# Performance work log

Hardware: AMD Instinct MI355X
Metric: run time of the kernel (lower is better)

The kernel has to match this reference:

```python
import jax, jax.numpy as jnp
import numpy as np

EPS = 1e-6

def _ln(x, g, b):
    m = jnp.mean(x, axis=-1, keepdims=True)
    v = jnp.mean(jnp.square(x - m), axis=-1, keepdims=True)
    return (x - m) * jax.lax.rsqrt(v + EPS) * g + b

def _pw(x, w, b):
    # 1x1 conv == channel matmul. x: [B,H,W,Ci], w: [Ci,Co]
    return jnp.einsum('bhwc,co->bhwo', x, w) + b

def _dw3x3(x, w, b):
    # depthwise 3x3, SAME. x: [B,H,W,C], w: [3,3,1,C]
    c = x.shape[-1]
    y = jax.lax.conv_general_dilated(
        x, w, window_strides=(1, 1), padding='SAME',
        dimension_numbers=('NHWC', 'HWIO', 'NHWC'),
        feature_group_count=c)
    return y + b

def setup_inputs() -> dict:
    key = jax.random.key(0)
    ks = jax.random.split(key, 16)
    B, H, W, C = 8, 256, 256, 64
    hid = C * 2            # channels * expansion
    s = lambda *sh: 0.02
    inp = {
        'x':     jax.random.normal(ks[0], (B, H, W, C), jnp.float32),
        'ln1_g': jnp.ones((C,), jnp.float32),
        'ln1_b': jnp.zeros((C,), jnp.float32),
        'pw1_w': jax.random.normal(ks[1], (C, hid * 2), jnp.float32) * 0.05,
        'pw1_b': jnp.zeros((hid * 2,), jnp.float32),
        'dw_w':  jax.random.normal(ks[2], (3, 3, 1, hid * 2), jnp.float32) * 0.05,
        'dw_b':  jnp.zeros((hid * 2,), jnp.float32),
        'sca_w': jax.random.normal(ks[3], (hid, hid), jnp.float32) * 0.05,
        'sca_b': jnp.zeros((hid,), jnp.float32),
        'pw2_w': jax.random.normal(ks[4], (hid, C), jnp.float32) * 0.05,
        'pw2_b': jnp.zeros((C,), jnp.float32),
        'beta':  jax.random.normal(ks[5], (1, 1, 1, C), jnp.float32) * 0.1,
        'ln2_g': jnp.ones((C,), jnp.float32),
        'ln2_b': jnp.zeros((C,), jnp.float32),
        'pw3_w': jax.random.normal(ks[6], (C, hid * 2), jnp.float32) * 0.05,
        'pw3_b': jnp.zeros((hid * 2,), jnp.float32),
        'pw4_w': jax.random.normal(ks[7], (hid, C), jnp.float32) * 0.05,
        'pw4_b': jnp.zeros((C,), jnp.float32),
        'gamma': jax.random.normal(ks[8], (1, 1, 1, C), jnp.float32) * 0.1,
    }
    return inp

def reference(x, ln1_g, ln1_b, pw1_w, pw1_b, dw_w, dw_b, sca_w, sca_b,
              pw2_w, pw2_b, beta, ln2_g, ln2_b, pw3_w, pw3_b, pw4_w, pw4_b, gamma):
    # ---- stage 1: norm -> pw1 -> dw3x3 -> SimpleGate -> SCA -> pw2 -> scaled residual
    y = _ln(x, ln1_g, ln1_b)
    y = _pw(y, pw1_w, pw1_b)            # [B,H,W,2*hid]
    y = _dw3x3(y, dw_w, dw_b)
    y1, y2 = jnp.split(y, 2, axis=-1)
    y = y1 * y2                          # SimpleGate -> [B,H,W,hid]
    w = jnp.mean(y, axis=(1, 2), keepdims=True)          # GAP [B,1,1,hid]
    w = _pw(w, sca_w, sca_b)             # 1x1 conv on pooled stats
    y = y * w                            # channel attention
    y = _pw(y, pw2_w, pw2_b)             # [B,H,W,C]
    x = x + y * beta
    # ---- stage 2: norm -> pw3 -> SimpleGate -> pw4 -> scaled residual
    z = _ln(x, ln2_g, ln2_b)
    z = _pw(z, pw3_w, pw3_b)             # [B,H,W,2*hid]
    z1, z2 = jnp.split(z, 2, axis=-1)
    z = z1 * z2                          # [B,H,W,hid]
    z = _pw(z, pw4_w, pw4_b)             # [B,H,W,C]
    return x + z * gamma
```

## Files before the change

kernel.cpp:

```cpp
#include <hip/hip_runtime.h>

typedef __attribute__((ext_vector_type(8))) _Float16 f16x8;
typedef __attribute__((ext_vector_type(2))) _Float16 h2;
typedef __attribute__((ext_vector_type(4))) float f32x4;
typedef __attribute__((ext_vector_type(2))) float f32x2;
typedef __attribute__((ext_vector_type(4))) unsigned uint4_t;
typedef __attribute__((ext_vector_type(2))) unsigned uint2_t;

__device__ __forceinline__ h2 pkrtz(float a, float b) {
    return __builtin_bit_cast(h2, __builtin_amdgcn_cvt_pkrtz(a, b));
}
__device__ __forceinline__ unsigned h2u(h2 v) { return __builtin_bit_cast(unsigned, v); }
__device__ __forceinline__ h2 u2h(unsigned u) { return __builtin_bit_cast(h2, u); }
__device__ __forceinline__ short f2h(float f) { return __builtin_bit_cast(short, (_Float16)f); }

#define OFF_W1T 0L
#define OFF_W2T 32768L
#define OFF_W3T 49152L
#define OFF_W4T 81920L
#define OFF_DWH 98304L
#define OFF_DBH 102912L
#define OFF_WATT 103424L
#define OFF_GPART 107520L
#define OFF_T 1156096L

__global__ __launch_bounds__(256) void k_prep(
    const float* __restrict__ w1, const float* __restrict__ w2,
    const float* __restrict__ w3, const float* __restrict__ w4,
    const float* __restrict__ dww, const float* __restrict__ dwb,
    short* __restrict__ w1t, short* __restrict__ w2t,
    short* __restrict__ w3t, short* __restrict__ w4t,
    short* __restrict__ dwh, short* __restrict__ dbh)
{
    int id = blockIdx.x * 256 + threadIdx.x;
    if (id < 64 * 256) {
        int ci = id >> 8, co = id & 255;
        w1t[co * 64 + ci] = f2h(w1[id]);
        w3t[co * 64 + ci] = f2h(w3[id]);
    }
    if (id < 128 * 64) {
        int ci = id >> 6, co = id & 63;
        w2t[co * 128 + ci] = f2h(w2[id]);
        w4t[co * 128 + ci] = f2h(w4[id]);
    }
    if (id < 9 * 256) dwh[id] = f2h(dww[id]);
    if (id < 256)     dbh[id] = f2h(dwb[id]);
}

__global__ __launch_bounds__(256) void k_a(
    const float* __restrict__ x, const float* __restrict__ ln1g, const float* __restrict__ ln1b,
    const short* __restrict__ w1t, const float* __restrict__ b1,
    const short* __restrict__ dwh, const short* __restrict__ dbh,
    short* __restrict__ t)
{
    __shared__ short uh[100 * 128];
    const int blk = blockIdx.x;
    const int cs  = blk & 1;
    const int txy = blk >> 1;
    const int tx  = txy & 31;
    const int ty  = (txy >> 5) & 31;
    const int b   = txy >> 10;
    const int tid = threadIdx.x;
    const int lane = tid & 63;
    const int wave = tid >> 6;
    const int m    = lane & 15;
    const int quad = lane >> 4;

    const int pA = wave * 16 + m;
    const int pB = pA + 64;
    const int hyA = (pA * 205) >> 11, hxA = pA - hyA * 10;
    const int hyB = (pB * 205) >> 11, hxB = pB - hyB * 10;
    const int gyA = ty * 8 + hyA - 1, gxA = tx * 8 + hxA - 1;
    const int gyB = ty * 8 + hyB - 1, gxB = tx * 8 + hxB - 1;
    const bool imgA = gyA >= 0 && gyA < 256 && gxA >= 0 && gxA < 256;
    const bool imgB = (pB < 100) && gyB >= 0 && gyB < 256 && gxB >= 0 && gxB < 256;
    const bool aliveB = (wave < 3);

    f32x4 fA[4], fB[4];
#pragma unroll
    for (int i = 0; i < 4; ++i) {
        fA[i] = (f32x4){0.f,0.f,0.f,0.f};
        fB[i] = (f32x4){0.f,0.f,0.f,0.f};
    }
    if (imgA) {
        const float* xr = x + ((long)((b * 256 + gyA) * 256 + gxA)) * 64 + quad * 8;
        fA[0] = *(const f32x4*)(xr);      fA[1] = *(const f32x4*)(xr + 4);
        fA[2] = *(const f32x4*)(xr + 32); fA[3] = *(const f32x4*)(xr + 36);
    }
    if (imgB) {
        const float* xr = x + ((long)((b * 256 + gyB) * 256 + gxB)) * 64 + quad * 8;
        fB[0] = *(const f32x4*)(xr);      fB[1] = *(const f32x4*)(xr + 4);
        fB[2] = *(const f32x4*)(xr + 32); fB[3] = *(const f32x4*)(xr + 36);
    }

    f32x4 g0 = *(const f32x4*)(ln1g + quad * 8);
    f32x4 g1 = *(const f32x4*)(ln1g + quad * 8 + 4);
    f32x4 g2 = *(const f32x4*)(ln1g + 32 + quad * 8);
    f32x4 g3 = *(const f32x4*)(ln1g + 32 + quad * 8 + 4);
    f32x4 c0 = *(const f32x4*)(ln1b + quad * 8);
    f32x4 c1 = *(const f32x4*)(ln1b + quad * 8 + 4);
    f32x4 c2 = *(const f32x4*)(ln1b + 32 + quad * 8);
    f32x4 c3 = *(const f32x4*)(ln1b + 32 + quad * 8 + 4);

    f16x8 a0A = {0,0,0,0,0,0,0,0}, a1A = {0,0,0,0,0,0,0,0};
    f16x8 a0B = {0,0,0,0,0,0,0,0}, a1B = {0,0,0,0,0,0,0,0};

    if (imgA) {
        float s  = 0.f, s2 = 0.f;
#pragma unroll
        for (int i = 0; i < 4; ++i)
#pragma unroll
            for (int r = 0; r < 4; ++r) { s += fA[i][r]; s2 += fA[i][r] * fA[i][r]; }
        s  += __shfl_xor(s, 16);  s  += __shfl_xor(s, 32);
        s2 += __shfl_xor(s2, 16); s2 += __shfl_xor(s2, 32);
        float mean = s * 0.015625f;
        float var  = s2 * 0.015625f - mean * mean;
        float rs   = rsqrtf(var + 1e-6f);
        float mrs  = mean * rs;
        uint4_t ra, rb;
#define LNP(va,vb,ga,gb,ca,cb) h2u(pkrtz(((va)*rs - mrs)*(ga) + (ca), ((vb)*rs - mrs)*(gb) + (cb)))
        ra[0] = LNP(fA[0][0],fA[0][1],g0[0],g0[1],c0[0],c0[1]);
        ra[1] = LNP(fA[0][2],fA[0][3],g0[2],g0[3],c0[2],c0[3]);
        ra[2] = LNP(fA[1][0],fA[1][1],g1[0],g1[1],c1[0],c1[1]);
        ra[3] = LNP(fA[1][2],fA[1][3],g1[2],g1[3],c1[2],c1[3]);
        rb[0] = LNP(fA[2][0],fA[2][1],g2[0],g2[1],c2[0],c2[1]);
        rb[1] = LNP(fA[2][2],fA[2][3],g2[2],g2[3],c2[2],c2[3]);
        rb[2] = LNP(fA[3][0],fA[3][1],g3[0],g3[1],c3[0],c3[1]);
        rb[3] = LNP(fA[3][2],fA[3][3],g3[2],g3[3],c3[2],c3[3]);
        a0A = __builtin_bit_cast(f16x8, ra);
        a1A = __builtin_bit_cast(f16x8, rb);
    }
    if (imgB) {
        float s  = 0.f, s2 = 0.f;
#pragma unroll
        for (int i = 0; i < 4; ++i)
#pragma unroll
            for (int r = 0; r < 4; ++r) { s += fB[i][r]; s2 += fB[i][r] * fB[i][r]; }
        s  += __shfl_xor(s, 16);  s  += __shfl_xor(s, 32);
        s2 += __shfl_xor(s2, 16); s2 += __shfl_xor(s2, 32);
        float mean = s * 0.015625f;
        float var  = s2 * 0.015625f - mean * mean;
        float rs   = rsqrtf(var + 1e-6f);
        float mrs  = mean * rs;
        uint4_t ra, rb;
        ra[0] = LNP(fB[0][0],fB[0][1],g0[0],g0[1],c0[0],c0[1]);
        ra[1] = LNP(fB[0][2],fB[0][3],g0[2],g0[3],c0[2],c0[3]);
        ra[2] = LNP(fB[1][0],fB[1][1],g1[0],g1[1],c1[0],c1[1]);
        ra[3] = LNP(fB[1][2],fB[1][3],g1[2],g1[3],c1[2],c1[3]);
        rb[0] = LNP(fB[2][0],fB[2][1],g2[0],g2[1],c2[0],c2[1]);
        rb[1] = LNP(fB[2][2],fB[2][3],g2[2],g2[3],c2[2],c2[3]);
        rb[2] = LNP(fB[3][0],fB[3][1],g3[0],g3[1],c3[0],c3[1]);
        rb[3] = LNP(fB[3][2],fB[3][3],g3[2],g3[3],c3[2],c3[3]);
#undef LNP
        a0B = __builtin_bit_cast(f16x8, ra);
        a1B = __builtin_bit_cast(f16x8, rb);
    }

    char* uhc = (char*)uh;
#pragma unroll
    for (int cot = 0; cot < 8; ++cot) {
        const int cob = (cot < 4) ? (cs * 64 + cot * 16) : (128 + cs * 64 + (cot - 4) * 16);
        const f16x8 wlo = __builtin_bit_cast(f16x8, *(const uint4_t*)(w1t + (cob + m) * 64 + quad * 8));
        const f16x8 whi = __builtin_bit_cast(f16x8, *(const uint4_t*)(w1t + (cob + m) * 64 + 32 + quad * 8));
        const f32x4 bv = *(const f32x4*)(b1 + cob + quad * 4);
        {
            f32x4 acc = {0.f,0.f,0.f,0.f};
            acc = __builtin_amdgcn_mfma_f32_16x16x32_f16(wlo, a0A, acc, 0, 0, 0);
            acc = __builtin_amdgcn_mfma_f32_16x16x32_f16(whi, a1A, acc, 0, 0, 0);
            uint2_t pk;
            pk[0] = imgA ? h2u(pkrtz(acc[0] + bv[0], acc[1] + bv[1])) : 0u;
            pk[1] = imgA ? h2u(pkrtz(acc[2] + bv[2], acc[3] + bv[3])) : 0u;
            int off = (pA * 256 + cot * 32 + quad * 8) ^ ((pA & 7) << 4);
            *(uint2_t*)(uhc + off) = pk;
        }
        if (aliveB) {
            f32x4 acc = {0.f,0.f,0.f,0.f};
            acc = __builtin_amdgcn_mfma_f32_16x16x32_f16(wlo, a0B, acc, 0, 0, 0);
            acc = __builtin_amdgcn_mfma_f32_16x16x32_f16(whi, a1B, acc, 0, 0, 0);
            if (pB < 100) {
                uint2_t pk;
                pk[0] = imgB ? h2u(pkrtz(acc[0] + bv[0], acc[1] + bv[1])) : 0u;
                pk[1] = imgB ? h2u(pkrtz(acc[2] + bv[2], acc[3] + bv[3])) : 0u;
                int off = (pB * 256 + cot * 32 + quad * 8) ^ ((pB & 7) << 4);
                *(uint2_t*)(uhc + off) = pk;
            }
        }
    }
    __syncthreads();

    const int y = lane >> 3, xx = lane & 7;
    const int cq = wave;
    const int gc0 = cs * 64 + cq * 16;
    const long gpx = ((long)(b * 256 + ty * 8 + y) * 256) + tx * 8 + xx;

    h2 A1[8], A2[8];
#pragma unroll
    for (int j = 0; j < 8; ++j) {
        A1[j] = u2h(0u);
        A2[j] = u2h(0u);
    }
#pragma unroll
    for (int dy = 0; dy < 3; ++dy)
#pragma unroll
    for (int dx = 0; dx < 3; ++dx) {
        int h = (y + dy) * 10 + (xx + dx);
        int sw = (h & 7) << 4;
        int b0 = h * 256 + cq * 32;
        uint4_t u1l  = *(const uint4_t*)(uhc + ((b0)       ^ sw));
        uint4_t u1h  = *(const uint4_t*)(uhc + ((b0 + 16)  ^ sw));
        uint4_t u2l  = *(const uint4_t*)(uhc + ((b0 + 128) ^ sw));
        uint4_t u2hv = *(const uint4_t*)(uhc + ((b0 + 144) ^ sw));
        const uint4_t* wp = (const uint4_t*)(dwh + (dy * 3 + dx) * 256 + gc0);
        const uint4_t* vp = (const uint4_t*)(dwh + (dy * 3 + dx) * 256 + 128 + gc0);
        uint4_t w1l = wp[0], w1h = wp[1];
        uint4_t w2l = vp[0], w2h = vp[1];
#pragma unroll
        for (int j = 0; j < 4; ++j) {
            A1[j]     += u2h(u1l[j])  * u2h(w1l[j]);
            A1[j + 4] += u2h(u1h[j])  * u2h(w1h[j]);
            A2[j]     += u2h(u2l[j])  * u2h(w2l[j]);
            A2[j + 4] += u2h(u2hv[j]) * u2h(w2h[j]);
        }
    }
    const uint4_t* bp1 = (const uint4_t*)(dbh + gc0);
    const uint4_t* bp2 = (const uint4_t*)(dbh + 128 + gc0);
    uint4_t b1l = bp1[0], b1h = bp1[1];
    uint4_t b2l = bp2[0], b2h = bp2[1];
    uint4_t s0, s1;
#pragma unroll
    for (int j = 0; j < 4; ++j) {
        h2 t0 = (A1[j]     + u2h(b1l[j])) * (A2[j]     + u2h(b2l[j]));
        h2 t1 = (A1[j + 4] + u2h(b1h[j])) * (A2[j + 4] + u2h(b2h[j]));
        s0[j] = h2u(t0);
        s1[j] = h2u(t1);
    }
    *(uint4_t*)(t + gpx * 128 + gc0)     = s0;
    *(uint4_t*)(t + gpx * 128 + gc0 + 8) = s1;
}

__global__ __launch_bounds__(256) void k_red(
    const short* __restrict__ t, float* __restrict__ gpart)
{
    __shared__ float red[16][16][8];
    const int blk = blockIdx.x;
    const int tid = threadIdx.x;
    const int cg = tid & 15;
    const int pr = tid >> 4;
    const short* tb = t + (long)blk * 256 * 128 + cg * 8;
    float a0=0,a1=0,a2=0,a3=0,a4=0,a5=0,a6=0,a7=0;
#pragma unroll 4
    for (int it = 0; it < 16; ++it) {
        uint4_t u = *(const uint4_t*)(tb + (long)(it * 16 + pr) * 128);
        h2 v0=u2h(u[0]), v1=u2h(u[1]), v2=u2h(u[2]), v3=u2h(u[3]);
        a0 += (float)v0[0]; a1 += (float)v0[1]; a2 += (float)v1[0]; a3 += (float)v1[1];
        a4 += (float)v2[0]; a5 += (float)v2[1]; a6 += (float)v3[0]; a7 += (float)v3[1];
    }
    red[pr][cg][0]=a0; red[pr][cg][1]=a1; red[pr][cg][2]=a2; red[pr][cg][3]=a3;
    red[pr][cg][4]=a4; red[pr][cg][5]=a5; red[pr][cg][6]=a6; red[pr][cg][7]=a7;
    __syncthreads();
    if (tid < 128) {
        int g = tid >> 3, j = tid & 7;
        float s = 0.f;
#pragma unroll
        for (int r = 0; r < 16; ++r) s += red[r][g][j];
        gpart[(long)blk * 128 + tid] = s;
    }
}

__global__ __launch_bounds__(256) void k_sca2(
    const float* __restrict__ gpart, const float* __restrict__ scaw,
    const float* __restrict__ scab, float* __restrict__ watt)
{
    __shared__ float gl[256];
    __shared__ float gn[128];
    const int b = blockIdx.x;
    const int tid = threadIdx.x;
    const int c = tid & 127, half = tid >> 7;
    float s = 0.f;
    const float* gp = gpart + (long)b * 256 * 128 + c;
    for (int i = half; i < 256; i += 2) s += gp[(long)i * 128];
    gl[half * 128 + c] = s;
    __syncthreads();
    if (tid < 128) gn[c] = (gl[c] + gl[128 + c]) * (1.0f / 65536.0f);
    __syncthreads();
    if (tid < 128) {
        float acc = scab[c];
        for (int ci = 0; ci < 128; ++ci) acc += gn[ci] * scaw[ci * 128 + c];
        watt[b * 128 + c] = acc;
    }
}

#define XLST 72
#define ZTST 136
__global__ __launch_bounds__(256) void k_b(
    const short* __restrict__ t, const float* __restrict__ watt,
    const short* __restrict__ w2t, const float* __restrict__ b2,
    const float* __restrict__ x, const float* __restrict__ beta,
    const float* __restrict__ ln2g, const float* __restrict__ ln2b,
    const short* __restrict__ w3t, const float* __restrict__ b3,
    const short* __restrict__ w4t, const float* __restrict__ b4,
    const float* __restrict__ gamma, float* __restrict__ out)
{
    __shared__ short xl[8][16 * XLST];
    __shared__ short zt[8][16 * ZTST];
    const int lane = threadIdx.x & 63;
    const int wave = threadIdx.x >> 6;
    const int m = lane & 15, quad = lane >> 4;
    const long pxA = (long)blockIdx.x * 128 + wave * 16 + m;
    const long pxB = pxA + 64;
    const int b = (int)(((long)blockIdx.x * 128) >> 16);
    const float* wa = watt + b * 128;
    const int sA = wave, sB = wave + 4;

    f32x4 xvA[4], xvB[4];
#pragma unroll
    for (int nt = 0; nt < 4; ++nt) {
        xvA[nt] = *(const f32x4*)(x + pxA * 64 + nt * 16 + quad * 4);
        xvB[nt] = *(const f32x4*)(x + pxB * 64 + nt * 16 + quad * 4);
    }

    const short* trA = t + pxA * 128;
    const short* trB = t + pxB * 128;
    f32x4 acc2A[4], acc2B[4];
#pragma unroll
    for (int nt = 0; nt < 4; ++nt) {
        acc2A[nt] = (f32x4){0.f,0.f,0.f,0.f};
        acc2B[nt] = (f32x4){0.f,0.f,0.f,0.f};
    }
#pragma unroll
    for (int kh = 0; kh < 4; ++kh) {
        uint4_t tA = *(const uint4_t*)(trA + kh * 32 + quad * 8);
        uint4_t tB = *(const uint4_t*)(trB + kh * 32 + quad * 8);
        f32x4 w0  = *(const f32x4*)(wa + kh * 32 + quad * 8);
        f32x4 w1v = *(const f32x4*)(wa + kh * 32 + quad * 8 + 4);
        h2 s01 = pkrtz(w0[0], w0[1]),  s23 = pkrtz(w0[2], w0[3]);
        h2 s45 = pkrtz(w1v[0], w1v[1]), s67 = pkrtz(w1v[2], w1v[3]);
        uint4_t oA, oB;
        oA[0] = h2u(u2h(tA[0]) * s01); oA[1] = h2u(u2h(tA[1]) * s23);
        oA[2] = h2u(u2h(tA[2]) * s45); oA[3] = h2u(u2h(tA[3]) * s67);
        oB[0] = h2u(u2h(tB[0]) * s01); oB[1] = h2u(u2h(tB[1]) * s23);
        oB[2] = h2u(u2h(tB[2]) * s45); oB[3] = h2u(u2h(tB[3]) * s67);
        f16x8 bfrA = __builtin_bit_cast(f16x8, oA);
        f16x8 bfrB = __builtin_bit_cast(f16x8, oB);
#pragma unroll
        for (int nt = 0; nt < 4; ++nt) {
            f16x8 aw = __builtin_bit_cast(f16x8,
                *(const uint4_t*)(w2t + (nt * 16 + m) * 128 + kh * 32 + quad * 8));
            acc2A[nt] = __builtin_amdgcn_mfma_f32_16x16x32_f16(aw, bfrA, acc2A[nt], 0, 0, 0);
            acc2B[nt] = __builtin_amdgcn_mfma_f32_16x16x32_f16(aw, bfrB, acc2B[nt], 0, 0, 0);
        }
    }
    float x1A[4][4], x1B[4][4];
#pragma unroll
    for (int nt = 0; nt < 4; ++nt) {
        int cob = nt * 16 + quad * 4;
        f32x4 bb = *(const f32x4*)(b2 + cob);
        f32x4 be = *(const f32x4*)(beta + cob);
#pragma unroll
        for (int r = 0; r < 4; ++r) {
            x1A[nt][r] = xvA[nt][r] + (acc2A[nt][r] + bb[r]) * be[r];
            x1B[nt][r] = xvB[nt][r] + (acc2B[nt][r] + bb[r]) * be[r];
        }
    }
    float sa = 0.f, s2a = 0.f, sb = 0.f, s2b = 0.f;
#pragma unroll
    for (int nt = 0; nt < 4; ++nt)
#pragma unroll
        for (int r = 0; r < 4; ++r) {
            sa += x1A[nt][r]; s2a += x1A[nt][r] * x1A[nt][r];
            sb += x1B[nt][r]; s2b += x1B[nt][r] * x1B[nt][r];
        }
    sa  += __shfl_xor(sa, 16);  sa  += __shfl_xor(sa, 32);
    s2a += __shfl_xor(s2a, 16); s2a += __shfl_xor(s2a, 32);
    sb  += __shfl_xor(sb, 16);  sb  += __shfl_xor(sb, 32);
    s2b += __shfl_xor(s2b, 16); s2b += __shfl_xor(s2b, 32);
    float meanA = sa * 0.015625f;
    float varA  = s2a * 0.015625f - meanA * meanA;
    float rsA   = rsqrtf(varA + 1e-6f);
    float mrsA  = meanA * rsA;
    float meanB = sb * 0.015625f;
    float varB  = s2b * 0.015625f - meanB * meanB;
    float rsB   = rsqrtf(varB + 1e-6f);
    float mrsB  = meanB * rsB;
#pragma unroll
    for (int nt = 0; nt < 4; ++nt) {
        int cob = nt * 16 + quad * 4;
        f32x4 gg = *(const f32x4*)(ln2g + cob);
        f32x4 cc = *(const f32x4*)(ln2b + cob);
        uint2_t pkA, pkB;
        pkA[0] = h2u(pkrtz((x1A[nt][0] * rsA - mrsA) * gg[0] + cc[0],
                           (x1A[nt][1] * rsA - mrsA) * gg[1] + cc[1]));
        pkA[1] = h2u(pkrtz((x1A[nt][2] * rsA - mrsA) * gg[2] + cc[2],
                           (x1A[nt][3] * rsA - mrsA) * gg[3] + cc[3]));
        pkB[0] = h2u(pkrtz((x1B[nt][0] * rsB - mrsB) * gg[0] + cc[0],
                           (x1B[nt][1] * rsB - mrsB) * gg[1] + cc[1]));
        pkB[1] = h2u(pkrtz((x1B[nt][2] * rsB - mrsB) * gg[2] + cc[2],
                           (x1B[nt][3] * rsB - mrsB) * gg[3] + cc[3]));
        *(uint2_t*)&xl[sA][m * XLST + cob] = pkA;
        *(uint2_t*)&xl[sB][m * XLST + cob] = pkB;
    }
    f16x8 xbA0 = __builtin_bit_cast(f16x8, *(const uint4_t*)&xl[sA][m * XLST + quad * 8]);
    f16x8 xbA1 = __builtin_bit_cast(f16x8, *(const uint4_t*)&xl[sA][m * XLST + 32 + quad * 8]);
    f16x8 xbB0 = __builtin_bit_cast(f16x8, *(const uint4_t*)&xl[sB][m * XLST + quad * 8]);
    f16x8 xbB1 = __builtin_bit_cast(f16x8, *(const uint4_t*)&xl[sB][m * XLST + 32 + quad * 8]);
#pragma unroll
    for (int pg = 0; pg < 8; ++pg) {
        f16x8 w3a0 = __builtin_bit_cast(f16x8, *(const uint4_t*)(w3t + (pg * 16 + m) * 64 + quad * 8));
        f16x8 w3a1 = __builtin_bit_cast(f16x8, *(const uint4_t*)(w3t + (pg * 16 + m) * 64 + 32 + quad * 8));
        f16x8 w3b0 = __builtin_bit_cast(f16x8, *(const uint4_t*)(w3t + (128 + pg * 16 + m) * 64 + quad * 8));
        f16x8 w3b1 = __builtin_bit_cast(f16x8, *(const uint4_t*)(w3t + (128 + pg * 16 + m) * 64 + 32 + quad * 8));
        f32x4 aAA = {0.f,0.f,0.f,0.f}, aBA = {0.f,0.f,0.f,0.f};
        f32x4 aAB = {0.f,0.f,0.f,0.f}, aBB = {0.f,0.f,0.f,0.f};
        aAA = __builtin_amdgcn_mfma_f32_16x16x32_f16(w3a0, xbA0, aAA, 0, 0, 0);
        aAA = __builtin_amdgcn_mfma_f32_16x16x32_f16(w3a1, xbA1, aAA, 0, 0, 0);
        aBA = __builtin_amdgcn_mfma_f32_16x16x32_f16(w3b0, xbA0, aBA, 0, 0, 0);
        aBA = __builtin_amdgcn_mfma_f32_16x16x32_f16(w3b1, xbA1, aBA, 0, 0, 0);
        aAB = __builtin_amdgcn_mfma_f32_16x16x32_f16(w3a0, xbB0, aAB, 0, 0, 0);
        aAB = __builtin_amdgcn_mfma_f32_16x16x32_f16(w3a1, xbB1, aAB, 0, 0, 0);
        aBB = __builtin_amdgcn_mfma_f32_16x16x32_f16(w3b0, xbB0, aBB, 0, 0, 0);
        aBB = __builtin_amdgcn_mfma_f32_16x16x32_f16(w3b1, xbB1, aBB, 0, 0, 0);
        int cb = pg * 16 + quad * 4;
        f32x4 bA_ = *(const f32x4*)(b3 + cb);
        f32x4 bB_ = *(const f32x4*)(b3 + 128 + cb);
        uint2_t pkA, pkB;
        pkA[0] = h2u(pkrtz((aAA[0] + bA_[0]) * (aBA[0] + bB_[0]),
                           (aAA[1] + bA_[1]) * (aBA[1] + bB_[1])));
        pkA[1] = h2u(pkrtz((aAA[2] + bA_[2]) * (aBA[2] + bB_[2]),
                           (aAA[3] + bA_[3]) * (aBA[3] + bB_[3])));
        pkB[0] = h2u(pkrtz((aAB[0] + bA_[0]) * (aBB[0] + bB_[0]),
                           (aAB[1] + bA_[1]) * (aBB[1] + bB_[1])));
        pkB[1] = h2u(pkrtz((aAB[2] + bA_[2]) * (aBB[2] + bB_[2]),
                           (aAB[3] + bA_[3]) * (aBB[3] + bB_[3])));
        *(uint2_t*)&zt[sA][m * ZTST + cb] = pkA;
        *(uint2_t*)&zt[sB][m * ZTST + cb] = pkB;
    }
    f32x4 acc4A[4], acc4B[4];
#pragma unroll
    for (int nt = 0; nt < 4; ++nt) {
        acc4A[nt] = (f32x4){0.f,0.f,0.f,0.f};
        acc4B[nt] = (f32x4){0.f,0.f,0.f,0.f};
    }
#pragma unroll
    for (int kh = 0; kh < 4; ++kh) {
        f16x8 zbA = __builtin_bit_cast(f16x8, *(const uint4_t*)&zt[sA][m * ZTST + kh * 32 + quad * 8]);
        f16x8 zbB = __builtin_bit_cast(f16x8, *(const uint4_t*)&zt[sB][m * ZTST + kh * 32 + quad * 8]);
#pragma unroll
        for (int nt = 0; nt < 4; ++nt) {
            f16x8 aw = __builtin_bit_cast(f16x8,
                *(const uint4_t*)(w4t + (nt * 16 + m) * 128 + kh * 32 + quad * 8));
            acc4A[nt] = __builtin_amdgcn_mfma_f32_16x16x32_f16(aw, zbA, acc4A[nt], 0, 0, 0);
            acc4B[nt] = __builtin_amdgcn_mfma_f32_16x16x32_f16(aw, zbB, acc4B[nt], 0, 0, 0);
        }
    }
#pragma unroll
    for (int nt = 0; nt < 4; ++nt) {
        int cob = nt * 16 + quad * 4;
        f32x4 bb = *(const f32x4*)(b4 + cob);
        f32x4 gm = *(const f32x4*)(gamma + cob);
        f32x4 oA, oB;
#pragma unroll
        for (int r = 0; r < 4; ++r) {
            oA[r] = x1A[nt][r] + (acc4A[nt][r] + bb[r]) * gm[r];
            oB[r] = x1B[nt][r] + (acc4B[nt][r] + bb[r]) * gm[r];
        }
        *(f32x4*)(out + pxA * 64 + cob) = oA;
        *(f32x4*)(out + pxB * 64 + cob) = oB;
    }
}

extern "C" void kernel_launch(void* const* d_in, const int* in_sizes, int n_in,
                              void* d_out, int out_size, void* d_ws, size_t ws_size,
                              hipStream_t stream) {
    (void)in_sizes; (void)n_in; (void)out_size; (void)ws_size;
    const float* x    = (const float*)d_in[0];
    const float* ln1g = (const float*)d_in[1];
    const float* ln1b = (const float*)d_in[2];
    const float* pw1w = (const float*)d_in[3];
    const float* pw1b = (const float*)d_in[4];
    const float* dww  = (const float*)d_in[5];
    const float* dwb  = (const float*)d_in[6];
    const float* scaw = (const float*)d_in[7];
    const float* scab = (const float*)d_in[8];
    const float* pw2w = (const float*)d_in[9];
    const float* pw2b = (const float*)d_in[10];
    const float* beta = (const float*)d_in[11];
    const float* ln2g = (const float*)d_in[12];
    const float* ln2b = (const float*)d_in[13];
    const float* pw3w = (const float*)d_in[14];
    const float* pw3b = (const float*)d_in[15];
    const float* pw4w = (const float*)d_in[16];
    const float* pw4b = (const float*)d_in[17];
    const float* gamma= (const float*)d_in[18];

    char* ws = (char*)d_ws;
    short* w1t = (short*)(ws + OFF_W1T);
    short* w2t = (short*)(ws + OFF_W2T);
    short* w3t = (short*)(ws + OFF_W3T);
    short* w4t = (short*)(ws + OFF_W4T);
    short* dwh = (short*)(ws + OFF_DWH);
    short* dbh = (short*)(ws + OFF_DBH);
    float* watt = (float*)(ws + OFF_WATT);
    float* gpart = (float*)(ws + OFF_GPART);
    short* t   = (short*)(ws + OFF_T);
    float* out = (float*)d_out;

    k_prep<<<64, 256, 0, stream>>>(pw1w, pw2w, pw3w, pw4w, dww, dwb,
                                   w1t, w2t, w3t, w4t, dwh, dbh);
    k_a<<<16384, 256, 0, stream>>>(x, ln1g, ln1b, w1t, pw1b, dwh, dbh, t);
    k_red<<<2048, 256, 0, stream>>>(t, gpart);
    k_sca2<<<8, 256, 0, stream>>>(gpart, scaw, scab, watt);
    k_b<<<4096, 256, 0, stream>>>(t, watt, w2t, pw2b, x, beta, ln2g, ln2b,
                                  w3t, pw3b, w4t, pw4b, gamma, out);
}
```

Measured before the change: 736.9 us.

## Fuse global-average-pool partial sums into k_a epilogue via wave shuffles

Each k_a wave now reduces its gated output across lanes with xor-shuffles and writes per-block channel partial sums. This replaces k_red, which re-read the whole fp16 intermediate tensor t from memory just to pool it. A small two-level reduction (k_red2, k_sca3) then combines the per-block partials before the SCA matmul. The trade is some extra shuffle work in k_a and fp16 accumulation within a wave, which may cost pooling precision.

```diff
diff --git a/kernel.cpp b/kernel.cpp
--- a/kernel.cpp
+++ b/kernel.cpp
@@ -22,7 +22,8 @@
 #define OFF_DBH 102912L
 #define OFF_WATT 103424L
 #define OFF_GPART 107520L
-#define OFF_T 1156096L
+#define OFF_GPART2 4301824L
+#define OFF_T 4334592L
 
 __global__ __launch_bounds__(256) void k_prep(
     const float* __restrict__ w1, const float* __restrict__ w2,
@@ -51,7 +52,7 @@
     const float* __restrict__ x, const float* __restrict__ ln1g, const float* __restrict__ ln1b,
     const short* __restrict__ w1t, const float* __restrict__ b1,
     const short* __restrict__ dwh, const short* __restrict__ dbh,
-    short* __restrict__ t)
+    short* __restrict__ t, float* __restrict__ gpart)
 {
     __shared__ short uh[100 * 128];
     const int blk = blockIdx.x;
@@ -236,57 +237,66 @@
     }
     *(uint4_t*)(t + gpx * 128 + gc0)     = s0;
     *(uint4_t*)(t + gpx * 128 + gc0 + 8) = s1;
-}
-
-__global__ __launch_bounds__(256) void k_red(
-    const short* __restrict__ t, float* __restrict__ gpart)
+
+#pragma unroll
+    for (int st = 1; st < 64; st <<= 1) {
+#pragma unroll
+        for (int j = 0; j < 4; ++j) {
+            s0[j] = h2u(u2h(s0[j]) + u2h((unsigned)__shfl_xor((int)s0[j], st)));
+            s1[j] = h2u(u2h(s1[j]) + u2h((unsigned)__shfl_xor((int)s1[j], st)));
+        }
+    }
+    if (lane == 0) {
+        float* gp = gpart + (long)blk * 64 + cq * 16;
+#pragma unroll
+        for (int j = 0; j < 4; ++j) {
+            h2 v0 = u2h(s0[j]), v1 = u2h(s1[j]);
+            f32x2 w0 = {(float)v0[0], (float)v0[1]};
+            f32x2 w1 = {(float)v1[0], (float)v1[1]};
+            *(f32x2*)(gp + 2 * j)     = w0;
+            *(f32x2*)(gp + 8 + 2 * j) = w1;
+        }
+    }
+}
+
+__global__ __launch_bounds__(256) void k_red2(
+    const float* __restrict__ gpart, float* __restrict__ gpart2)
 {
-    __shared__ float red[16][16][8];
-    const int blk = blockIdx.x;
+    __shared__ float red[2][128];
+    const int b = blockIdx.x >> 3;
+    const int sg = blockIdx.x & 7;
     const int tid = threadIdx.x;
-    const int cg = tid & 15;
-    const int pr = tid >> 4;
-    const short* tb = t + (long)blk * 256 * 128 + cg * 8;
-    float a0=0,a1=0,a2=0,a3=0,a4=0,a5=0,a6=0,a7=0;
+    const int c = tid & 127, h = tid >> 7;
+    const int cs = c >> 6, lc = c & 63;
+    float acc = 0.f;
 #pragma unroll 4
-    for (int it = 0; it < 16; ++it) {
-        uint4_t u = *(const uint4_t*)(tb + (long)(it * 16 + pr) * 128);
-        h2 v0=u2h(u[0]), v1=u2h(u[1]), v2=u2h(u[2]), v3=u2h(u[3]);
-        a0 += (float)v0[0]; a1 += (float)v0[1]; a2 += (float)v1[0]; a3 += (float)v1[1];
-        a4 += (float)v2[0]; a5 += (float)v2[1]; a6 += (float)v3[0]; a7 += (float)v3[1];
-    }
-    red[pr][cg][0]=a0; red[pr][cg][1]=a1; red[pr][cg][2]=a2; red[pr][cg][3]=a3;
-    red[pr][cg][4]=a4; red[pr][cg][5]=a5; red[pr][cg][6]=a6; red[pr][cg][7]=a7;
+    for (int i = 0; i < 64; ++i) {
+        int txy = sg * 128 + h * 64 + i;
+        acc += gpart[((long)(b * 1024 + txy) * 2 + cs) * 64 + lc];
+    }
+    red[h][c] = acc;
     __syncthreads();
-    if (tid < 128) {
-        int g = tid >> 3, j = tid & 7;
-        float s = 0.f;
-#pragma unroll
-        for (int r = 0; r < 16; ++r) s += red[r][g][j];
-        gpart[(long)blk * 128 + tid] = s;
-    }
-}
-
-__global__ __launch_bounds__(256) void k_sca2(
-    const float* __restrict__ gpart, const float* __restrict__ scaw,
+    if (tid < 128) gpart2[(b * 8 + sg) * 128 + c] = red[0][c] + red[1][c];
+}
+
+__global__ __launch_bounds__(256) void k_sca3(
+    const float* __restrict__ gpart2, const float* __restrict__ scaw,
     const float* __restrict__ scab, float* __restrict__ watt)
 {
-    __shared__ float gl[256];
     __shared__ float gn[128];
     const int b = blockIdx.x;
     const int tid = threadIdx.x;
-    const int c = tid & 127, half = tid >> 7;
-    float s = 0.f;
-    const float* gp = gpart + (long)b * 256 * 128 + c;
-    for (int i = half; i < 256; i += 2) s += gp[(long)i * 128];
-    gl[half * 128 + c] = s;
-    __syncthreads();
-    if (tid < 128) gn[c] = (gl[c] + gl[128 + c]) * (1.0f / 65536.0f);
+    if (tid < 128) {
+        float s = 0.f;
+#pragma unroll
+        for (int sg = 0; sg < 8; ++sg) s += gpart2[(b * 8 + sg) * 128 + tid];
+        gn[tid] = s * (1.0f / 65536.0f);
+    }
     __syncthreads();
     if (tid < 128) {
-        float acc = scab[c];
-        for (int ci = 0; ci < 128; ++ci) acc += gn[ci] * scaw[ci * 128 + c];
-        watt[b * 128 + c] = acc;
+        float acc = scab[tid];
+        for (int ci = 0; ci < 128; ++ci) acc += gn[ci] * scaw[ci * 128 + tid];
+        watt[b * 128 + tid] = acc;
     }
 }
 
@@ -501,14 +511,15 @@
     short* dbh = (short*)(ws + OFF_DBH);
     float* watt = (float*)(ws + OFF_WATT);
     float* gpart = (float*)(ws + OFF_GPART);
+    float* gpart2 = (float*)(ws + OFF_GPART2);
     short* t   = (short*)(ws + OFF_T);
     float* out = (float*)d_out;
 
     k_prep<<<64, 256, 0, stream>>>(pw1w, pw2w, pw3w, pw4w, dww, dwb,
                                    w1t, w2t, w3t, w4t, dwh, dbh);
-    k_a<<<16384, 256, 0, stream>>>(x, ln1g, ln1b, w1t, pw1b, dwh, dbh, t);
-    k_red<<<2048, 256, 0, stream>>>(t, gpart);
-    k_sca2<<<8, 256, 0, stream>>>(gpart, scaw, scab, watt);
+    k_a<<<16384, 256, 0, stream>>>(x, ln1g, ln1b, w1t, pw1b, dwh, dbh, t, gpart);
+    k_red2<<<64, 256, 0, stream>>>(gpart, gpart2);
+    k_sca3<<<8, 256, 0, stream>>>(gpart2, scaw, scab, watt);
     k_b<<<4096, 256, 0, stream>>>(t, watt, w2t, pw2b, x, beta, ln2g, ln2b,
                                   w3t, pw3b, w4t, pw4b, gamma, out);
 }
```

Measured after the change: 697.4 us. -5.4%, faster.
